# Kernel tuning notes

Measured on AMD Instinct MI355X. Metric: run time of the kernel, lower is better.

The kernel has to match this reference:

```python
import jax, jax.numpy as jnp
import numpy as np

LN_EPS = 1e-5
EPS = 1e-8
NUM_ITERS = 3

def _ln(x, w, b):
    mu = jnp.mean(x, axis=-1, keepdims=True)
    var = jnp.var(x, axis=-1, keepdims=True)
    return (x - mu) * jax.lax.rsqrt(var + LN_EPS) * w + b

def setup_inputs() -> dict:
    key = jax.random.key(0)
    ks = jax.random.split(key, 20)
    B, H, W, C = 16, 64, 64, 256
    D, S, HID, T = 128, 10, 256, 20
    g = lambda k, *shape: jax.random.normal(k, shape, dtype=jnp.float32) * 0.02
    return {
        'obs': jax.random.normal(ks[0], (B, H, W, C), dtype=jnp.float32),
        'noise': jax.random.normal(ks[1], (B, S, D), dtype=jnp.float32),
        'slots_mu': jax.random.normal(ks[2], (1, 1, D), dtype=jnp.float32),
        'slots_log_sigma': jax.random.normal(ks[3], (1, 1, D), dtype=jnp.float32) * 0.1,
        'ni_w': jnp.ones((C,), jnp.float32), 'ni_b': jnp.zeros((C,), jnp.float32),
        'ns_w': jnp.ones((D,), jnp.float32), 'ns_b': jnp.zeros((D,), jnp.float32),
        'nm_w': jnp.ones((D,), jnp.float32), 'nm_b': jnp.zeros((D,), jnp.float32),
        'Wq': g(ks[4], D, D), 'Wk': g(ks[5], C, D), 'Wv': g(ks[6], C, D),
        'mlp_w1': g(ks[7], D, 2 * D), 'mlp_b1': jnp.zeros((2 * D,), jnp.float32),
        'mlp_w2': g(ks[8], 2 * D, D), 'mlp_b2': jnp.zeros((D,), jnp.float32),
        'pd_w1': g(ks[9], D, HID), 'pd_b1': jnp.zeros((HID,), jnp.float32),
        'pd_w2': g(ks[10], HID, D), 'pd_b2': jnp.zeros((D,), jnp.float32),
        'tc_w': g(ks[11], D, T), 'tc_b': jnp.zeros((T,), jnp.float32),
    }

def reference(obs, noise, slots_mu, slots_log_sigma, ni_w, ni_b, ns_w, ns_b,
              nm_w, nm_b, Wq, Wk, Wv, mlp_w1, mlp_b1, mlp_w2, mlp_b2,
              pd_w1, pd_b1, pd_w2, pd_b2, tc_w, tc_b):
    B = obs.shape[0]
    x = obs.reshape(B, -1, obs.shape[-1])  # [B, N, C] (flatten H,W)
    D = Wq.shape[0]
    # slot init: mu + sigma * noise
    slots = slots_mu + jnp.exp(slots_log_sigma) * noise  # [B, S, D]
    x = _ln(x, ni_w, ni_b)
    k = x @ Wk  # [B, N, D]
    v = x @ Wv  # [B, N, D]
    scale = D ** -0.5
    attn = None
    for _ in range(NUM_ITERS):
        slots_prev = slots
        q = _ln(slots, ns_w, ns_b) @ Wq  # [B, S, D]
        logits = jnp.einsum('bsd,bnd->bsn', q, k) * scale
        attn = jax.nn.softmax(logits, axis=1)  # competitive over slots
        w = attn / (jnp.sum(attn, axis=-1, keepdims=True) + EPS)
        updates = jnp.einsum('bsn,bnd->bsd', w, v)
        slots = slots_prev + updates
        h = _ln(slots, nm_w, nm_b)
        slots = slots + (jax.nn.relu(h @ mlp_w1 + mlp_b1) @ mlp_w2 + mlp_b2)
    objects = jax.nn.relu(slots @ pd_w1 + pd_b1) @ pd_w2 + pd_b2
    object_types = slots @ tc_w + tc_b
    return objects, object_types
```

## Files before the change

### kernel.cpp

```cpp
#include <hip/hip_runtime.h>
#include <hip/hip_bf16.h>

typedef __hip_bfloat16 bf16;
typedef __attribute__((ext_vector_type(8))) short bf16x8;
typedef __attribute__((ext_vector_type(4))) float f32x4;

#define LN_EPS 1e-5f
#define ATT_EPS 1e-8f

__device__ __forceinline__ float bflo(unsigned u){ union{unsigned i;float f;}c; c.i=u<<16; return c.f; }
__device__ __forceinline__ float bfhi(unsigned u){ union{unsigned i;float f;}c; c.i=u&0xffff0000u; return c.f; }
__device__ __forceinline__ float bf2f(bf16 h){ return __bfloat162float(h); }
__device__ __forceinline__ unsigned f2bfbits(float f){
    bf16 h = __float2bfloat16(f);
    unsigned short s; __builtin_memcpy(&s, &h, 2);
    return (unsigned)s;
}
__device__ __forceinline__ int detect_isf(const void* niw){
    unsigned u0; __builtin_memcpy(&u0, niw, 4);
    return (u0 == 0x3F800000u) ? 1 : 0;
}

__device__ __forceinline__ float getv(const void* p, long i, int isf){
    if (isf) return ((const float*)p)[i];
    return bf2f(((const bf16*)p)[i]);
}
__device__ __forceinline__ void get8(const void* p, long i, int isf, float* o){
    if (isf){
        __builtin_memcpy(o, (const float*)p + i, 32);
    } else {
        unsigned u[4];
        __builtin_memcpy(u, (const bf16*)p + i, 16);
        o[0]=bflo(u[0]); o[1]=bfhi(u[0]); o[2]=bflo(u[1]); o[3]=bfhi(u[1]);
        o[4]=bflo(u[2]); o[5]=bfhi(u[2]); o[6]=bflo(u[3]); o[7]=bfhi(u[3]);
    }
}
__device__ __forceinline__ void load4f(const float* p, float* o){ __builtin_memcpy(o, p, 16); }
__device__ __forceinline__ void store4f(float* p, const float* v){ __builtin_memcpy(p, v, 16); }

__device__ __forceinline__ void wred2(float& a, float& b){
    #pragma unroll
    for (int m = 32; m > 0; m >>= 1){
        a += __shfl_xor(a, m, 64);
        b += __shfl_xor(b, m, 64);
    }
}

__device__ __forceinline__ void phaseD2(
        int b, int s, int t, const float* shlns,
        const void* __restrict__ Wq, const void* __restrict__ Wk,
        const void* __restrict__ niw, const void* __restrict__ nib, int isf,
        bf16* __restrict__ wkqb, float* __restrict__ Ug, float* __restrict__ Vg,
        float* __restrict__ P2, float* __restrict__ t0g, float* __restrict__ t1g,
        float* redQ, float* qsh, float* redUV){
    {
        int g = t & 15, ks = t >> 4;
        float a8[8] = {0,0,0,0,0,0,0,0};
        #pragma unroll
        for (int j = 0; j < 8; j++){
            int d = ks*8 + j;
            float w8[8]; get8(Wq, (long)d*128 + g*8, isf, w8);
            float pv = shlns[d];
            #pragma unroll
            for (int k = 0; k < 8; k++) a8[k] += pv*w8[k];
        }
        store4f(&redQ[ks*128 + g*8], a8);
        store4f(&redQ[ks*128 + g*8 + 4], a8+4);
    }
    __syncthreads();
    if (t < 128){
        float qv = 0.f;
        #pragma unroll
        for (int ks = 0; ks < 16; ks++) qv += redQ[ks*128 + t];
        qsh[t] = qv * 0.08838834764831845f;
    }
    __syncthreads();
    int c = t;
    float kqc = 0.f;
    for (int d0 = 0; d0 < 128; d0 += 8){
        float w8[8]; get8(Wk, (long)c*128 + d0, isf, w8);
        float qa[4], qb[4]; load4f(qsh + d0, qa); load4f(qsh + d0 + 4, qb);
        kqc += w8[0]*qa[0]+w8[1]*qa[1]+w8[2]*qa[2]+w8[3]*qa[3]
             + w8[4]*qb[0]+w8[5]*qb[1]+w8[6]*qb[2]+w8[7]*qb[3];
    }
    float wc = getv(niw, c, isf), bc = getv(nib, c, isf);
    float wkq = wc*kqc, vq = bc*kqc;
    float uu = wkq, vv = vq;
    wred2(uu, vv);
    int wid = t >> 6, lane = t & 63;
    if (lane == 0){ redUV[wid*2] = uu; redUV[wid*2+1] = vv; }
    wkqb[((long)b*16 + s)*256 + c] = __float2bfloat16(wkq);
    int bsI = b*10 + s;
    P2[bsI*256 + c] = 0.f;
    __syncthreads();
    if (t == 0){
        Ug[bsI] = redUV[0] + redUV[2] + redUV[4] + redUV[6];
        Vg[bsI] = redUV[1] + redUV[3] + redUV[5] + redUV[7];
        t0g[bsI] = 0.f; t1g[bsI] = 0.f;
    }
}

__global__ __launch_bounds__(256) void k_prep(
        const void* __restrict__ noise, const void* __restrict__ smu,
        const void* __restrict__ sls, const void* __restrict__ nsw,
        const void* __restrict__ nsb, const void* __restrict__ niw,
        const void* __restrict__ nib, const void* __restrict__ Wq,
        const void* __restrict__ Wk, float* __restrict__ slots,
        bf16* __restrict__ wkqb, float* __restrict__ Ug, float* __restrict__ Vg,
        float* __restrict__ P2, float* __restrict__ t0g, float* __restrict__ t1g){
    int isf = detect_isf(niw);
    int bs = blockIdx.x, t = threadIdx.x;
    int b = bs/10, s = bs - b*10;
    __shared__ __align__(16) float shlns[128];
    __shared__ __align__(16) float redQ[16*128];
    __shared__ __align__(16) float qsh[128];
    __shared__ float red[2][2];
    __shared__ float redUV[8];
    if (t < 128){
        float sv = getv(smu,t,isf) + __expf(getv(sls,t,isf)) * getv(noise,(long)bs*128+t,isf);
        slots[bs*128 + t] = sv;
        shlns[t] = sv;
        float su = sv, sq = sv*sv;
        wred2(su, sq);
        int wid = t >> 6, lane = t & 63;
        if (lane == 0){ red[wid][0]=su; red[wid][1]=sq; }
    }
    __syncthreads();
    if (t < 128){
        float su = red[0][0]+red[1][0], sq = red[0][1]+red[1][1];
        float m = su*(1.f/128.f), var = sq*(1.f/128.f) - m*m;
        float ri = rsqrtf(var + LN_EPS);
        shlns[t] = (shlns[t] - m)*ri*getv(nsw,t,isf) + getv(nsb,t,isf);
    }
    __syncthreads();
    phaseD2(b, s, t, shlns, Wq, Wk, niw, nib, isf, wkqb, Ug, Vg, P2, t0g, t1g,
            redQ, qsh, redUV);
    if (s == 0){
        #pragma unroll
        for (int r = 10; r < 16; r++)
            wkqb[((long)b*16 + r)*256 + t] = __float2bfloat16(0.f);
    }
}

__global__ __launch_bounds__(256) void k_attn6(
        const void* __restrict__ obs, const bf16* __restrict__ wkqb,
        const float* __restrict__ Ug, const float* __restrict__ Vg,
        const void* __restrict__ niw, float* __restrict__ P2,
        float* __restrict__ t0g, float* __restrict__ t1g){
    int isf = detect_isf(niw);
    int tile = blockIdx.x, b = blockIdx.y, t = threadIdx.x;
    int w = t >> 6, l = t & 63;
    __shared__ unsigned sxn[64*132];
    __shared__ __align__(16) float attnP[64*16];
    __shared__ float muri[128];
    __shared__ float denp0[4][16], denp1[4][16];

    if (isf){
        const float* gx = (const float*)obs + ((long)b*4096 + tile*64)*256;
        #pragma unroll
        for (int i = 0; i < 8; i++){
            int Ld = t*4 + i*1024;
            int px = Ld >> 7, col = Ld & 127;
            float f8[8];
            __builtin_memcpy(f8, gx + (long)px*256 + col*2, 32);
            unsigned pk[4];
            #pragma unroll
            for (int k2=0;k2<4;k2++)
                pk[k2] = (f2bfbits(f8[2*k2+1])<<16) | f2bfbits(f8[2*k2]);
            __builtin_memcpy(&sxn[px*132 + col], pk, 16);
        }
    } else {
        const unsigned* gx = (const unsigned*)obs + ((long)b*4096 + tile*64)*128;
        #pragma unroll
        for (int i = 0; i < 8; i++){
            int Ld = t*4 + i*1024;
            int px = Ld >> 7, col = Ld & 127;
            unsigned tmp[4];
            __builtin_memcpy(tmp, gx + Ld, 16);
            __builtin_memcpy(&sxn[px*132 + col], tmp, 16);
        }
    }
    bf16x8 bfr[8];
    {
        int s = l & 15, q = (l >> 4) & 3;
        const bf16* base = wkqb + ((long)b*16 + s)*256 + q*8;
        #pragma unroll
        for (int ks = 0; ks < 8; ks++)
            __builtin_memcpy(&bfr[ks], base + ks*32, 16);
    }
    __syncthreads();

    {
        int px = t >> 2, q = t & 3;
        float su = 0.f, sq = 0.f;
        #pragma unroll
        for (int j = 0; j < 8; j++){
            unsigned d4[4];
            __builtin_memcpy(d4, &sxn[px*132 + q*32 + j*4], 16);
            #pragma unroll
            for (int k2=0;k2<4;k2++){
                float a0 = bflo(d4[k2]), a1 = bfhi(d4[k2]);
                su += a0 + a1; sq += a0*a0 + a1*a1;
            }
        }
        su += __shfl_xor(su,1,64); sq += __shfl_xor(sq,1,64);
        su += __shfl_xor(su,2,64); sq += __shfl_xor(sq,2,64);
        if (q == 0){
            float m = su*(1.f/256.f);
            float ri = rsqrtf(sq*(1.f/256.f) - m*m + LN_EPS);
            muri[px*2] = m; muri[px*2+1] = ri;
        }
    }
    __syncthreads();

    f32x4 acc = {0.f,0.f,0.f,0.f};
    {
        int m = l & 15, q = (l >> 4) & 3;
        int rowbase = (w*16 + m)*132;
        #pragma unroll
        for (int ks = 0; ks < 8; ks++){
            bf16x8 af;
            __builtin_memcpy(&af, &sxn[rowbase + ks*16 + q*4], 16);
            acc = __builtin_amdgcn_mfma_f32_16x16x32_bf16(af, bfr[ks], acc, 0, 0, 0);
        }
    }

    {
        int col = l & 15, q = (l >> 4) & 3;
        float Uv = 0.f, Vv = 0.f;
        if (col < 10){ Uv = Ug[b*10 + col]; Vv = Vg[b*10 + col]; }
        float pden0 = 0.f, pden1 = 0.f;
        #pragma unroll
        for (int reg = 0; reg < 4; reg++){
            int px = w*16 + q*4 + reg;
            float mr[2]; __builtin_memcpy(mr, &muri[px*2], 8);
            float lg = (col < 10) ? (mr[1]*acc[reg] - mr[1]*mr[0]*Uv + Vv) : -1e30f;
            float mx = lg;
            mx = fmaxf(mx, __shfl_xor(mx,1,64));
            mx = fmaxf(mx, __shfl_xor(mx,2,64));
            mx = fmaxf(mx, __shfl_xor(mx,4,64));
            mx = fmaxf(mx, __shfl_xor(mx,8,64));
            float e = (col < 10) ? __expf(lg - mx) : 0.f;
            float sm = e;
            sm += __shfl_xor(sm,1,64);
            sm += __shfl_xor(sm,2,64);
            sm += __shfl_xor(sm,4,64);
            sm += __shfl_xor(sm,8,64);
            float a = e / sm;
            attnP[px*16 + col] = a*mr[1];
            pden0 += a;
            pden1 += a*mr[1]*mr[0];
        }
        pden0 += __shfl_xor(pden0,16,64); pden0 += __shfl_xor(pden0,32,64);
        pden1 += __shfl_xor(pden1,16,64); pden1 += __shfl_xor(pden1,32,64);
        if (l < 10){ denp0[w][l] = pden0; denp1[w][l] = pden1; }
    }
    __syncthreads();
    if (t < 10){
        atomicAdd(&t0g[b*10 + t], denp0[0][t]+denp0[1][t]+denp0[2][t]+denp0[3][t]);
        atomicAdd(&t1g[b*10 + t], denp1[0][t]+denp1[1][t]+denp1[2][t]+denp1[3][t]);
    }

    {
        int col = l & 15, q = (l >> 4) & 3;
        bf16x8 afr[2];
        #pragma unroll
        for (int ks = 0; ks < 2; ks++){
            short tmpa[8];
            #pragma unroll
            for (int j = 0; j < 8; j++){
                int px = ks*32 + q*8 + j;
                tmpa[j] = (short)f2bfbits(attnP[px*16 + col]);
            }
            __builtin_memcpy(&afr[ks], tmpa, 16);
        }
        const unsigned short* xs = (const unsigned short*)sxn;
        #pragma unroll
        for (int nt = 0; nt < 4; nt++){
            int cfull = w*64 + nt*16 + col;
            f32x4 c2 = {0.f,0.f,0.f,0.f};
            #pragma unroll
            for (int ks = 0; ks < 2; ks++){
                short tmpb[8];
                #pragma unroll
                for (int j = 0; j < 8; j++){
                    int px = ks*32 + q*8 + j;
                    tmpb[j] = (short)xs[px*264 + cfull];
                }
                bf16x8 bf_;
                __builtin_memcpy(&bf_, tmpb, 16);
                c2 = __builtin_amdgcn_mfma_f32_16x16x32_bf16(afr[ks], bf_, c2, 0, 0, 0);
            }
            #pragma unroll
            for (int reg = 0; reg < 4; reg++){
                int s = q*4 + reg;
                if (s < 10)
                    atomicAdd(&P2[b*2560 + s*256 + cfull], c2[reg]);
            }
        }
    }
}

__global__ __launch_bounds__(256) void k_slot(
        float* __restrict__ slots, float* __restrict__ P2,
        float* __restrict__ t0g, float* __restrict__ t1g,
        const void* __restrict__ Wv,
        const void* __restrict__ nmw, const void* __restrict__ nmb,
        const void* __restrict__ w1, const void* __restrict__ b1,
        const void* __restrict__ w2, const void* __restrict__ b2,
        const void* __restrict__ nsw, const void* __restrict__ nsb,
        const void* __restrict__ niw, const void* __restrict__ nib,
        const void* __restrict__ Wq, const void* __restrict__ Wk,
        const void* __restrict__ pw1, const void* __restrict__ pb1,
        const void* __restrict__ pw2, const void* __restrict__ pb2,
        const void* __restrict__ tw, const void* __restrict__ tb,
        bf16* __restrict__ wkqb, float* __restrict__ Ug, float* __restrict__ Vg,
        void* __restrict__ out, int last){
    int isf = detect_isf(niw);
    int bs = blockIdx.x, t = threadIdx.x;
    int b = bs/10, s = bs - b*10;
    __shared__ __align__(16) float pr[256];
    __shared__ __align__(16) float redA[16*128];
    __shared__ __align__(16) float redB[8*256];
    __shared__ __align__(16) float redT[8*32];
    __shared__ __align__(16) float hld[128];
    __shared__ __align__(16) float hid[256];
    __shared__ __align__(16) float shlns[128];
    __shared__ __align__(16) float qsh[128];
    __shared__ float red[4][2];
    __shared__ float redUV[8];

    float t0v = t0g[bs], t1v = t1g[bs];
    float wc = getv(niw,t,isf), bcv = getv(nib,t,isf);
    pr[t] = (P2[bs*256 + t] - t1v)*wc + t0v*bcv;
    __syncthreads();

    {
        int g = t & 15, ks = t >> 4;
        int d0 = g*8;
        float a8[8] = {0,0,0,0,0,0,0,0};
        #pragma unroll
        for (int j=0;j<16;j++){
            int c2 = ks*16 + j;
            float w8[8]; get8(Wv, (long)c2*128 + d0, isf, w8);
            float pv = pr[c2];
            #pragma unroll
            for (int k=0;k<8;k++) a8[k] += pv*w8[k];
        }
        store4f(&redA[ks*128 + d0], a8);
        store4f(&redA[ks*128 + d0 + 4], a8+4);
    }
    __syncthreads();
    float dv = t0v + ATT_EPS;
    float sn = 0.f;
    if (t < 128){
        float u = 0.f;
        #pragma unroll
        for (int ks=0;ks<16;ks++) u += redA[ks*128 + t];
        sn = slots[bs*128 + t] + u/dv;
    }
    float v = (t < 128) ? sn : 0.f;
    float su = v, sq = v*v;
    wred2(su, sq);
    int wid = t >> 6, lane = t & 63;
    if (lane == 0){ red[wid][0]=su; red[wid][1]=sq; }
    __syncthreads();
    su = red[0][0]+red[1][0]+red[2][0]+red[3][0];
    sq = red[0][1]+red[1][1]+red[2][1]+red[3][1];
    float mu = su*(1.f/128.f), var = sq*(1.f/128.f) - mu*mu;
    float rinv = rsqrtf(var + LN_EPS);
    if (t < 128) hld[t] = (v-mu)*rinv*getv(nmw,t,isf) + getv(nmb,t,isf);
    __syncthreads();

    {
        int g = t & 31, ks = t >> 5;
        int h0 = g*8;
        float a8[8] = {0,0,0,0,0,0,0,0};
        #pragma unroll
        for (int j=0;j<16;j++){
            int d = ks*16 + j;
            float w8[8]; get8(w1, (long)d*256 + h0, isf, w8);
            float hv = hld[d];
            #pragma unroll
            for (int k=0;k<8;k++) a8[k] += hv*w8[k];
        }
        store4f(&redB[ks*256 + h0], a8);
        store4f(&redB[ks*256 + h0 + 4], a8+4);
    }
    __syncthreads();
    {
        float hb = getv(b1,t,isf);
        #pragma unroll
        for (int ks=0;ks<8;ks++) hb += redB[ks*256 + t];
        hid[t] = fmaxf(hb, 0.f);
    }
    __syncthreads();

    {
        int g = t & 15, ks = t >> 4;
        int d0 = g*8;
        float a8[8] = {0,0,0,0,0,0,0,0};
        #pragma unroll
        for (int j=0;j<16;j++){
            int h = ks*16 + j;
            float w8[8]; get8(w2, (long)h*128 + d0, isf, w8);
            float hv = hid[h];
            #pragma unroll
            for (int k=0;k<8;k++) a8[k] += hv*w8[k];
        }
        store4f(&redA[ks*128 + d0], a8);
        store4f(&redA[ks*128 + d0 + 4], a8+4);
    }
    __syncthreads();
    float v2 = 0.f;
    if (t < 128){
        float o = getv(b2,t,isf);
        #pragma unroll
        for (int ks=0;ks<16;ks++) o += redA[ks*128 + t];
        v2 = sn + o;
    }

    if (!last){
        if (t < 128) slots[bs*128 + t] = v2;
        float s2 = v2, ss2 = v2*v2;
        wred2(s2, ss2);
        if (lane == 0){ red[wid][0]=s2; red[wid][1]=ss2; }
        __syncthreads();
        s2 = red[0][0]+red[1][0]+red[2][0]+red[3][0];
        ss2 = red[0][1]+red[1][1]+red[2][1]+red[3][1];
        float mu2 = s2*(1.f/128.f), var2 = ss2*(1.f/128.f) - mu2*mu2;
        float ri2 = rsqrtf(var2 + LN_EPS);
        if (t < 128)
            shlns[t] = (v2 - mu2)*ri2*getv(nsw,t,isf) + getv(nsb,t,isf);
        __syncthreads();
        phaseD2(b, s, t, shlns, Wq, Wk, niw, nib, isf, wkqb, Ug, Vg, P2, t0g, t1g,
                redA, qsh, redUV);
    } else {
        if (t < 128) shlns[t] = v2;
        __syncthreads();
        {
            int g = t & 31, ks = t >> 5;
            int h0 = g*8;
            float a8[8] = {0,0,0,0,0,0,0,0};
            #pragma unroll
            for (int j=0;j<16;j++){
                int d = ks*16 + j;
                float w8[8]; get8(pw1, (long)d*256 + h0, isf, w8);
                float hv = shlns[d];
                #pragma unroll
                for (int k=0;k<8;k++) a8[k] += hv*w8[k];
            }
            store4f(&redB[ks*256 + h0], a8);
            store4f(&redB[ks*256 + h0 + 4], a8+4);
        }
        __syncthreads();
        {
            float hb = getv(pb1,t,isf);
            #pragma unroll
            for (int ks=0;ks<8;ks++) hb += redB[ks*256 + t];
            hid[t] = fmaxf(hb, 0.f);
        }
        __syncthreads();
        {
            int g = t & 15, ks = t >> 4;
            int d0 = g*8;
            float a8[8] = {0,0,0,0,0,0,0,0};
            #pragma unroll
            for (int j=0;j<16;j++){
                int h = ks*16 + j;
                float w8[8]; get8(pw2, (long)h*128 + d0, isf, w8);
                float hv = hid[h];
                #pragma unroll
                for (int k=0;k<8;k++) a8[k] += hv*w8[k];
            }
            store4f(&redA[ks*128 + d0], a8);
            store4f(&redA[ks*128 + d0 + 4], a8+4);
        }
        {
            int ot = t & 31, ks = t >> 5;
            float a = 0.f;
            if (ot < 20){
                #pragma unroll
                for (int j=0;j<16;j++){
                    int d = ks*16 + j;
                    a += shlns[d]*getv(tw, (long)d*20 + ot, isf);
                }
            }
            redT[ks*32 + ot] = a;
        }
        __syncthreads();
        if (t < 128){
            float o = getv(pb2,t,isf);
            #pragma unroll
            for (int ks=0;ks<16;ks++) o += redA[ks*128 + t];
            int idx = bs*128 + t;
            if (isf) ((float*)out)[idx] = o; else ((bf16*)out)[idx] = __float2bfloat16(o);
        }
        if (t < 20){
            float o = getv(tb,t,isf);
            #pragma unroll
            for (int ks=0;ks<8;ks++) o += redT[ks*32 + t];
            int idx = 16*10*128 + bs*20 + t;
            if (isf) ((float*)out)[idx] = o; else ((bf16*)out)[idx] = __float2bfloat16(o);
        }
    }
}

extern "C" void kernel_launch(void* const* d_in, const int* in_sizes, int n_in,
                              void* d_out, int out_size, void* d_ws, size_t ws_size,
                              hipStream_t stream) {
    const void* obs   = d_in[0];
    const void* noise = d_in[1];
    const void* smu   = d_in[2];
    const void* sls   = d_in[3];
    const void* niw   = d_in[4];
    const void* nib   = d_in[5];
    const void* nsw   = d_in[6];
    const void* nsb   = d_in[7];
    const void* nmw   = d_in[8];
    const void* nmb   = d_in[9];
    const void* Wq    = d_in[10];
    const void* Wk    = d_in[11];
    const void* Wv    = d_in[12];
    const void* w1    = d_in[13];
    const void* b1    = d_in[14];
    const void* w2    = d_in[15];
    const void* b2    = d_in[16];
    const void* pw1   = d_in[17];
    const void* pb1   = d_in[18];
    const void* pw2   = d_in[19];
    const void* pb2   = d_in[20];
    const void* tw    = d_in[21];
    const void* tb    = d_in[22];

    char* ws = (char*)d_ws;
    float* t0g   = (float*)(ws);
    float* t1g   = (float*)(ws + 1024);
    float* Ug    = (float*)(ws + 2048);
    float* Vg    = (float*)(ws + 3072);
    float* slots = (float*)(ws + 4096);
    float* P2    = (float*)(ws + 86016);
    bf16*  wkqb  = (bf16*) (ws + 249856);

    k_prep<<<160, 256, 0, stream>>>(noise, smu, sls, nsw, nsb, niw, nib, Wq, Wk,
                                    slots, wkqb, Ug, Vg, P2, t0g, t1g);
    for (int it = 0; it < 3; it++){
        k_attn6<<<dim3(64, 16), 256, 0, stream>>>(obs, wkqb, Ug, Vg, niw, P2, t0g, t1g);
        k_slot<<<160, 256, 0, stream>>>(slots, P2, t0g, t1g, Wv, nmw, nmb,
                                        w1, b1, w2, b2, nsw, nsb, niw, nib,
                                        Wq, Wk, pw1, pb1, pw2, pb2, tw, tb,
                                        wkqb, Ug, Vg, d_out, (it == 2) ? 1 : 0);
    }
}
```

Measured before the change: 243.1 us.

## Fuse slot-update kernel into attention kernel via last-arriving-block tail

The separate k_slot launch is removed. Each attention block now writes its per-tile partial products to a dedicated buffer instead of doing atomicAdd into P2, then bumps a per-batch ticket counter. The last ten arriving blocks of each batch spin until all 64 tiles have arrived. Each of those ten then sums the 64 partials for one slot and runs the slot MLP, LayerNorm and next-query prep, reusing the tile's shared memory. This removes three kernel launches and the float atomics, at the cost of a spin-wait, a serial 64-way reduction per thread, and a dependency on forward progress of co-resident blocks.

```diff
diff --git a/kernel.cpp b/kernel.cpp
--- a/kernel.cpp
+++ b/kernel.cpp
@@ -51,7 +51,7 @@
         const void* __restrict__ Wq, const void* __restrict__ Wk,
         const void* __restrict__ niw, const void* __restrict__ nib, int isf,
         bf16* __restrict__ wkqb, float* __restrict__ Ug, float* __restrict__ Vg,
-        float* __restrict__ P2, float* __restrict__ t0g, float* __restrict__ t1g,
+        float* __restrict__ t0g, float* __restrict__ t1g,
         float* redQ, float* qsh, float* redUV){
     {
         int g = t & 15, ks = t >> 4;
@@ -91,7 +91,6 @@
     if (lane == 0){ redUV[wid*2] = uu; redUV[wid*2+1] = vv; }
     wkqb[((long)b*16 + s)*256 + c] = __float2bfloat16(wkq);
     int bsI = b*10 + s;
-    P2[bsI*256 + c] = 0.f;
     __syncthreads();
     if (t == 0){
         Ug[bsI] = redUV[0] + redUV[2] + redUV[4] + redUV[6];
@@ -107,7 +106,7 @@
         const void* __restrict__ nib, const void* __restrict__ Wq,
         const void* __restrict__ Wk, float* __restrict__ slots,
         bf16* __restrict__ wkqb, float* __restrict__ Ug, float* __restrict__ Vg,
-        float* __restrict__ P2, float* __restrict__ t0g, float* __restrict__ t1g){
+        float* __restrict__ t0g, float* __restrict__ t1g, int* __restrict__ tick){
     int isf = detect_isf(niw);
     int bs = blockIdx.x, t = threadIdx.x;
     int b = bs/10, s = bs - b*10;
@@ -116,6 +115,7 @@
     __shared__ __align__(16) float qsh[128];
     __shared__ float red[2][2];
     __shared__ float redUV[8];
+    if (bs == 0 && t < 48) tick[t] = 0;
     if (t < 128){
         float sv = getv(smu,t,isf) + __expf(getv(sls,t,isf)) * getv(noise,(long)bs*128+t,isf);
         slots[bs*128 + t] = sv;
@@ -133,7 +133,7 @@
         shlns[t] = (shlns[t] - m)*ri*getv(nsw,t,isf) + getv(nsb,t,isf);
     }
     __syncthreads();
-    phaseD2(b, s, t, shlns, Wq, Wk, niw, nib, isf, wkqb, Ug, Vg, P2, t0g, t1g,
+    phaseD2(b, s, t, shlns, Wq, Wk, niw, nib, isf, wkqb, Ug, Vg, t0g, t1g,
             redQ, qsh, redUV);
     if (s == 0){
         #pragma unroll
@@ -142,18 +142,30 @@
     }
 }
 
-__global__ __launch_bounds__(256) void k_attn6(
-        const void* __restrict__ obs, const bf16* __restrict__ wkqb,
-        const float* __restrict__ Ug, const float* __restrict__ Vg,
-        const void* __restrict__ niw, float* __restrict__ P2,
-        float* __restrict__ t0g, float* __restrict__ t1g){
+__global__ __launch_bounds__(256) void k_attn7(
+        const void* __restrict__ obs, bf16* __restrict__ wkqb,
+        float* __restrict__ Ug, float* __restrict__ Vg,
+        const void* __restrict__ niw, const void* __restrict__ nib,
+        float* __restrict__ t0g, float* __restrict__ t1g,
+        float* __restrict__ pp, int* __restrict__ tick,
+        float* __restrict__ slots, const void* __restrict__ Wv,
+        const void* __restrict__ nmw, const void* __restrict__ nmb,
+        const void* __restrict__ w1, const void* __restrict__ b1,
+        const void* __restrict__ w2, const void* __restrict__ b2,
+        const void* __restrict__ nsw, const void* __restrict__ nsb,
+        const void* __restrict__ Wq, const void* __restrict__ Wk,
+        const void* __restrict__ pw1, const void* __restrict__ pb1,
+        const void* __restrict__ pw2, const void* __restrict__ pb2,
+        const void* __restrict__ tw, const void* __restrict__ tb,
+        void* __restrict__ out, int last){
     int isf = detect_isf(niw);
     int tile = blockIdx.x, b = blockIdx.y, t = threadIdx.x;
     int w = t >> 6, l = t & 63;
-    __shared__ unsigned sxn[64*132];
+    __shared__ __align__(16) unsigned sxn[64*132];
     __shared__ __align__(16) float attnP[64*16];
     __shared__ float muri[128];
     __shared__ float denp0[4][16], denp1[4][16];
+    __shared__ int sret;
 
     if (isf){
         const float* gx = (const float*)obs + ((long)b*4096 + tile*64)*256;
@@ -295,44 +307,45 @@
             for (int reg = 0; reg < 4; reg++){
                 int s = q*4 + reg;
                 if (s < 10)
-                    atomicAdd(&P2[b*2560 + s*256 + cfull], c2[reg]);
-            }
-        }
-    }
-}
-
-__global__ __launch_bounds__(256) void k_slot(
-        float* __restrict__ slots, float* __restrict__ P2,
-        float* __restrict__ t0g, float* __restrict__ t1g,
-        const void* __restrict__ Wv,
-        const void* __restrict__ nmw, const void* __restrict__ nmb,
-        const void* __restrict__ w1, const void* __restrict__ b1,
-        const void* __restrict__ w2, const void* __restrict__ b2,
-        const void* __restrict__ nsw, const void* __restrict__ nsb,
-        const void* __restrict__ niw, const void* __restrict__ nib,
-        const void* __restrict__ Wq, const void* __restrict__ Wk,
-        const void* __restrict__ pw1, const void* __restrict__ pb1,
-        const void* __restrict__ pw2, const void* __restrict__ pb2,
-        const void* __restrict__ tw, const void* __restrict__ tb,
-        bf16* __restrict__ wkqb, float* __restrict__ Ug, float* __restrict__ Vg,
-        void* __restrict__ out, int last){
-    int isf = detect_isf(niw);
-    int bs = blockIdx.x, t = threadIdx.x;
-    int b = bs/10, s = bs - b*10;
-    __shared__ __align__(16) float pr[256];
-    __shared__ __align__(16) float redA[16*128];
-    __shared__ __align__(16) float redB[8*256];
-    __shared__ __align__(16) float redT[8*32];
-    __shared__ __align__(16) float hld[128];
-    __shared__ __align__(16) float hid[256];
-    __shared__ __align__(16) float shlns[128];
-    __shared__ __align__(16) float qsh[128];
-    __shared__ float red[4][2];
-    __shared__ float redUV[8];
-
+                    pp[(((long)b*10 + s)*64 + tile)*256 + cfull] = c2[reg];
+            }
+        }
+    }
+
+    __threadfence();
+    if (t == 0) sret = atomicAdd(&tick[b], 1);
+    __syncthreads();
+    int ret = sret;
+    if (ret < 54) return;
+    int s = ret - 54;
+    if (t == 0){
+        while (__hip_atomic_load(&tick[b], __ATOMIC_ACQUIRE, __HIP_MEMORY_SCOPE_AGENT) < 64)
+            __builtin_amdgcn_s_sleep(8);
+    }
+    __syncthreads();
+    __threadfence();
+
+    char* sm = (char*)sxn;
+    float* pr    = (float*)sm;
+    float* redA  = (float*)(sm + 1024);
+    float* redB  = (float*)(sm + 9216);
+    float* redT  = (float*)(sm + 17408);
+    float* hld   = (float*)(sm + 18432);
+    float* hid   = (float*)(sm + 18944);
+    float* shlns = (float*)(sm + 19968);
+    float* qsh   = (float*)(sm + 20480);
+    float* redS  = (float*)(sm + 20992);
+    float* redUV = (float*)(sm + 21024);
+
+    int bs = b*10 + s;
     float t0v = t0g[bs], t1v = t1g[bs];
     float wc = getv(niw,t,isf), bcv = getv(nib,t,isf);
-    pr[t] = (P2[bs*256 + t] - t1v)*wc + t0v*bcv;
+    {
+        float accp = 0.f;
+        const float* ppb = pp + (long)bs*64*256 + t;
+        for (int t2 = 0; t2 < 64; t2++) accp += ppb[t2*256];
+        pr[t] = (accp - t1v)*wc + t0v*bcv;
+    }
     __syncthreads();
 
     {
@@ -363,10 +376,10 @@
     float su = v, sq = v*v;
     wred2(su, sq);
     int wid = t >> 6, lane = t & 63;
-    if (lane == 0){ red[wid][0]=su; red[wid][1]=sq; }
-    __syncthreads();
-    su = red[0][0]+red[1][0]+red[2][0]+red[3][0];
-    sq = red[0][1]+red[1][1]+red[2][1]+red[3][1];
+    if (lane == 0){ redS[wid*2]=su; redS[wid*2+1]=sq; }
+    __syncthreads();
+    su = redS[0]+redS[2]+redS[4]+redS[6];
+    sq = redS[1]+redS[3]+redS[5]+redS[7];
     float mu = su*(1.f/128.f), var = sq*(1.f/128.f) - mu*mu;
     float rinv = rsqrtf(var + LN_EPS);
     if (t < 128) hld[t] = (v-mu)*rinv*getv(nmw,t,isf) + getv(nmb,t,isf);
@@ -424,16 +437,16 @@
         if (t < 128) slots[bs*128 + t] = v2;
         float s2 = v2, ss2 = v2*v2;
         wred2(s2, ss2);
-        if (lane == 0){ red[wid][0]=s2; red[wid][1]=ss2; }
+        if (lane == 0){ redS[wid*2]=s2; redS[wid*2+1]=ss2; }
         __syncthreads();
-        s2 = red[0][0]+red[1][0]+red[2][0]+red[3][0];
-        ss2 = red[0][1]+red[1][1]+red[2][1]+red[3][1];
+        s2 = redS[0]+redS[2]+redS[4]+redS[6];
+        ss2 = redS[1]+redS[3]+redS[5]+redS[7];
         float mu2 = s2*(1.f/128.f), var2 = ss2*(1.f/128.f) - mu2*mu2;
         float ri2 = rsqrtf(var2 + LN_EPS);
         if (t < 128)
             shlns[t] = (v2 - mu2)*ri2*getv(nsw,t,isf) + getv(nsb,t,isf);
         __syncthreads();
-        phaseD2(b, s, t, shlns, Wq, Wk, niw, nib, isf, wkqb, Ug, Vg, P2, t0g, t1g,
+        phaseD2(b, s, t, shlns, Wq, Wk, niw, nib, isf, wkqb, Ug, Vg, t0g, t1g,
                 redA, qsh, redUV);
     } else {
         if (t < 128) shlns[t] = v2;
@@ -538,17 +551,17 @@
     float* t1g   = (float*)(ws + 1024);
     float* Ug    = (float*)(ws + 2048);
     float* Vg    = (float*)(ws + 3072);
-    float* slots = (float*)(ws + 4096);
-    float* P2    = (float*)(ws + 86016);
-    bf16*  wkqb  = (bf16*) (ws + 249856);
+    int*   tick  = (int*)  (ws + 4096);
+    float* slots = (float*)(ws + 4352);
+    bf16*  wkqb  = (bf16*) (ws + 86272);
+    float* pp    = (float*)(ws + 217344);
 
     k_prep<<<160, 256, 0, stream>>>(noise, smu, sls, nsw, nsb, niw, nib, Wq, Wk,
-                                    slots, wkqb, Ug, Vg, P2, t0g, t1g);
+                                    slots, wkqb, Ug, Vg, t0g, t1g, tick);
     for (int it = 0; it < 3; it++){
-        k_attn6<<<dim3(64, 16), 256, 0, stream>>>(obs, wkqb, Ug, Vg, niw, P2, t0g, t1g);
-        k_slot<<<160, 256, 0, stream>>>(slots, P2, t0g, t1g, Wv, nmw, nmb,
-                                        w1, b1, w2, b2, nsw, nsb, niw, nib,
-                                        Wq, Wk, pw1, pb1, pw2, pb2, tw, tb,
-                                        wkqb, Ug, Vg, d_out, (it == 2) ? 1 : 0);
-    }
-}
+        k_attn7<<<dim3(64, 16), 256, 0, stream>>>(
+            obs, wkqb, Ug, Vg, niw, nib, t0g, t1g, pp, tick + it*16,
+            slots, Wv, nmw, nmb, w1, b1, w2, b2, nsw, nsb, Wq, Wk,
+            pw1, pb1, pw2, pb2, tw, tb, d_out, (it == 2) ? 1 : 0);
+    }
+}
```

Result: slower. 843.8 us (+247.1%).
